# Kernel optimization log

Measured on AMD Instinct MI355X. Metric: run time of the kernel, lower is better.

## Reference

```python
import jax, jax.numpy as jnp
import numpy as np

B, S, D, H = 16, 1024, 768, 12
HD = D // H  # head_dim = 64

def setup_inputs() -> dict:
    key = jax.random.key(0)
    ks = jax.random.split(key, 6)
    s = 1.0 / np.sqrt(D)
    return {
        "z": jax.random.normal(ks[0], (B, S, D), dtype=jnp.float32),
        "W_q": jax.random.normal(ks[1], (D, D), dtype=jnp.float32) * s,
        "W_k": jax.random.normal(ks[2], (D, D), dtype=jnp.float32) * s,
        "W_v": jax.random.normal(ks[3], (D, D), dtype=jnp.float32) * s,
        "W_o": jax.random.normal(ks[4], (D, D), dtype=jnp.float32) * s,
        "b_o": jax.random.normal(ks[5], (D,), dtype=jnp.float32) * s,
    }

def reference(z, W_q, W_k, W_v, W_o, b_o):
    batch, seq, _ = z.shape
    # torch Linear: y = x @ W.T
    q = (z @ W_q.T).reshape(batch, seq, H, HD).transpose(0, 2, 1, 3)  # [B,H,S,hd]
    k = (z @ W_k.T).reshape(batch, seq, H, HD).transpose(0, 2, 1, 3)
    v = (z @ W_v.T).reshape(batch, seq, H, HD).transpose(0, 2, 1, 3)
    scores = jnp.einsum("bhqd,bhkd->bhqk", q, k) / np.sqrt(HD)
    attn = jax.nn.softmax(scores, axis=-1)
    ctx = jnp.einsum("bhqk,bhkd->bhqd", attn, v)  # [B,H,S,hd]
    ctx = ctx.transpose(0, 2, 1, 3).reshape(batch, seq, D)
    return ctx @ W_o.T + b_o
```

## Files before the change

kernel.cpp:

```cpp
#include <hip/hip_runtime.h>
#include <hip/hip_bf16.h>


typedef __attribute__((ext_vector_type(4))) float f32x4;
typedef __attribute__((ext_vector_type(16))) float f32x16;
typedef __attribute__((ext_vector_type(8))) __bf16 bf16x8;
typedef __attribute__((ext_vector_type(4))) unsigned int u32x4;

#if __has_builtin(__builtin_amdgcn_exp2f)
#define EXP2F __builtin_amdgcn_exp2f
#else
#define EXP2F exp2f
#endif

__device__ __forceinline__ unsigned short f2bf(float f) {
  union { float f; unsigned u; } v; v.f = f;
  unsigned r = v.u + 0x7FFFu + ((v.u >> 16) & 1u);
  return (unsigned short)(r >> 16);
}

__device__ __forceinline__ unsigned cvtpk(float a, float b) {
  unsigned r;
  asm("v_cvt_pk_bf16_f32 %0, %1, %2" : "=v"(r) : "v"(a), "v"(b));
  return r;
}

__device__ __forceinline__ void gl_lds16(const void* g, void* l) {
  __builtin_amdgcn_global_load_lds(
      (const __attribute__((address_space(1))) void*)g,
      (__attribute__((address_space(3))) void*)l, 16, 0, 0);
}

__global__ void cvt_f32_bf16(const float* __restrict__ in,
                             unsigned short* __restrict__ out, int n4) {
  int i = blockIdx.x * blockDim.x + threadIdx.x;
  int stride = gridDim.x * blockDim.x;
  for (; i < n4; i += stride) {
    float4 v = ((const float4*)in)[i];
    ushort4 o;
    o.x = f2bf(v.x); o.y = f2bf(v.y); o.z = f2bf(v.z); o.w = f2bf(v.w);
    ((ushort4*)out)[i] = o;
  }
}

__global__ void cvt4_f32_bf16(const float* __restrict__ i0, const float* __restrict__ i1,
                              const float* __restrict__ i2, const float* __restrict__ i3,
                              unsigned short* __restrict__ o0, unsigned short* __restrict__ o1,
                              unsigned short* __restrict__ o2, unsigned short* __restrict__ o3,
                              int n4) {
  const float* in = (blockIdx.y == 0) ? i0 : (blockIdx.y == 1) ? i1 : (blockIdx.y == 2) ? i2 : i3;
  unsigned short* out = (blockIdx.y == 0) ? o0 : (blockIdx.y == 1) ? o1 : (blockIdx.y == 2) ? o2 : o3;
  int i = blockIdx.x * blockDim.x + threadIdx.x;
  int stride = gridDim.x * blockDim.x;
  for (; i < n4; i += stride) {
    float4 v = ((const float4*)in)[i];
    ushort4 o;
    o.x = f2bf(v.x); o.y = f2bf(v.y); o.z = f2bf(v.z); o.w = f2bf(v.w);
    ((ushort4*)out)[i] = o;
  }
}

__global__ __launch_bounds__(256) void qkv_gemm(
    const unsigned short* __restrict__ A,
    const unsigned short* __restrict__ Wq,
    const unsigned short* __restrict__ Wk,
    const unsigned short* __restrict__ Wv,
    unsigned short* __restrict__ Qo,
    unsigned short* __restrict__ Ko,
    unsigned short* __restrict__ Vt) {
  __shared__ unsigned short As[2][128 * 64];
  __shared__ unsigned short Bs[2][128 * 64];
  const int bid = blockIdx.x;
  const int xcd = bid & 7, slot = bid >> 3;
  const int mt = xcd * 16 + slot / 18;
  const int rem = slot % 18;
  const int which = rem / 6;
  const int nt = rem % 6;
  const unsigned short* __restrict__ W =
      (which == 0) ? Wq : (which == 1) ? Wk : Wv;
  const int m0 = mt * 128;
  const int n0 = nt * 128;
  const int tid = threadIdx.x;
  const int lane = tid & 63;
  const int l15 = lane & 15, lg = lane >> 4;
  const int w = tid >> 6;
  const int wm = (w >> 1) * 64, wn = (w & 1) * 64;

  const int srow = tid >> 3;
  const int scg8 = (((tid & 7) ^ (srow & 7)) << 3);

#define QSTAGE(bi, kt)                                                         \
  do {                                                                         \
    _Pragma("unroll") for (int it = 0; it < 4; ++it) {                         \
      int row = srow + it * 32;                                                \
      int dst = (row * 8 + (tid & 7)) * 8;                                     \
      gl_lds16(A + (size_t)(m0 + row) * 768 + (kt) + scg8, &As[bi][dst]);      \
      gl_lds16(W + (size_t)(n0 + row) * 768 + (kt) + scg8, &Bs[bi][dst]);      \
    }                                                                          \
  } while (0)

  f32x4 acc[4][4] = {};
  const int rxf = l15 & 7;

  QSTAGE(0, 0);
  for (int kt = 0; kt < 768; kt += 64) {
    const int cur = (kt >> 6) & 1;
    if (kt < 704) {
      QSTAGE(cur ^ 1, kt + 64);
      asm volatile("s_waitcnt vmcnt(8)" ::: "memory");
    } else {
      asm volatile("s_waitcnt vmcnt(0)" ::: "memory");
    }
    __builtin_amdgcn_s_barrier();
    __builtin_amdgcn_sched_barrier(0);
#pragma unroll
    for (int kk = 0; kk < 64; kk += 32) {
      const int g0 = kk >> 3;
      bf16x8 a[4], b[4];
#pragma unroll
      for (int i = 0; i < 4; ++i)
        a[i] = *(const bf16x8*)&As[cur][(wm + i * 16 + l15) * 64 + (((g0 + lg) ^ rxf) << 3)];
#pragma unroll
      for (int j = 0; j < 4; ++j)
        b[j] = *(const bf16x8*)&Bs[cur][(wn + j * 16 + l15) * 64 + (((g0 + lg) ^ rxf) << 3)];
#pragma unroll
      for (int i = 0; i < 4; ++i)
#pragma unroll
        for (int j = 0; j < 4; ++j)
          acc[i][j] = __builtin_amdgcn_mfma_f32_16x16x32_bf16(
              a[i], b[j], acc[i][j], 0, 0, 0);
    }
    asm volatile("s_waitcnt lgkmcnt(0)" ::: "memory");
    __builtin_amdgcn_sched_barrier(0);
    __builtin_amdgcn_s_barrier();
  }

  if (which < 2) {
    unsigned short* __restrict__ O = which == 0 ? Qo : Ko;
    const float scl = which == 0 ? 0.125f * 1.44269504088896f : 1.0f;
#pragma unroll
    for (int i = 0; i < 4; ++i)
#pragma unroll
      for (int j = 0; j < 4; ++j)
#pragma unroll
        for (int r = 0; r < 4; ++r) {
          int row = m0 + wm + i * 16 + lg * 4 + r;
          int col = n0 + wn + j * 16 + l15;
          O[(size_t)row * 768 + col] = f2bf(acc[i][j][r] * scl);
        }
  } else {
#pragma unroll
    for (int i = 0; i < 4; ++i)
#pragma unroll
      for (int j = 0; j < 4; ++j) {
        int m = m0 + wm + i * 16 + lg * 4;
        int bb = m >> 10, s = m & 1023;
        int col = n0 + wn + j * 16 + l15;
        size_t off = ((size_t)(bb * 12 + (col >> 6)) * 64 + (col & 63)) * 1024 + s;
        ushort4 pk;
        pk.x = f2bf(acc[i][j][0]);
        pk.y = f2bf(acc[i][j][1]);
        pk.z = f2bf(acc[i][j][2]);
        pk.w = f2bf(acc[i][j][3]);
        *(ushort4*)(Vt + off) = pk;
      }
  }
#undef QSTAGE
}

__global__ __launch_bounds__(256, 2) void attn_fwd(
    const unsigned short* __restrict__ Q,
    const unsigned short* __restrict__ K,
    const unsigned short* __restrict__ Vt,
    unsigned short* __restrict__ ctx) {
  __shared__ unsigned short Ks[4][64 * 64];
  __shared__ unsigned short Vs[4][64 * 64];
  const int wg = blockIdx.x;
  const int xcd = wg & 7, slot = wg >> 3;
  const int bh = xcd * 24 + (slot >> 2);
  const int qt = slot & 3;
  const int b = bh / 12, h = bh - b * 12;

  const int tid = threadIdx.x;
  const int lane = tid & 63;
  const int l31 = lane & 31;
  const int hi = lane >> 5;
  const int w = tid >> 6;
  const int qbase = qt * 256 + w * 64;

  const size_t qkoff = (size_t)b * (1024 * 768) + h * 64;
  const size_t vtoff = (size_t)bh * (64 * 1024);

  const int sc = lane & 7;
  const int srsub = lane >> 3;
  const int scg = sc ^ srsub;
  const int srow0 = w * 16 + srsub;

  const unsigned short* k0 = K + qkoff + scg * 8 + (size_t)srow0 * 768;
  const unsigned short* k1 = k0 + 8 * 768;
  const unsigned short* v0 = Vt + vtoff + scg * 8 + (size_t)srow0 * 1024;
  const unsigned short* v1 = v0 + 8 * 1024;
  const int d0 = srow0 * 64 + sc * 8;
  const int d1 = d0 + 8 * 64;

#define STAGE(bi)                                                              \
  do {                                                                         \
    gl_lds16(k0, &Ks[bi][d0]);                                                 \
    gl_lds16(k1, &Ks[bi][d1]);                                                 \
    gl_lds16(v0, &Vs[bi][d0]);                                                 \
    gl_lds16(v1, &Vs[bi][d1]);                                                 \
    k0 += 64 * 768; k1 += 64 * 768; v0 += 64; v1 += 64;                        \
  } while (0)

  bf16x8 bqA[4], bqB[4];
  const unsigned short* Qp = Q + qkoff + (size_t)(qbase + l31) * 768 + hi * 8;
#pragma unroll
  for (int ks = 0; ks < 4; ++ks) {
    bqA[ks] = *(const bf16x8*)(Qp + ks * 16);
    bqB[ks] = *(const bf16x8*)(Qp + 32 * 768 + ks * 16);
  }

  f32x16 oA0 = {}, oA1 = {}, oB0 = {}, oB1 = {};
  float laccA[8] = {}, laccB[8] = {};

  const int rxor = l31 & 7;

#define ATTN_BODY(buf)                                                         \
  do {                                                                         \
    bf16x8 ak[2][4], bv[2][4];                                                 \
    _Pragma("unroll") for (int kb2 = 0; kb2 < 2; ++kb2)                        \
      _Pragma("unroll") for (int ks = 0; ks < 4; ++ks)                         \
        ak[kb2][ks] = *(const bf16x8*)&Ks[buf][(kb2 * 32 + l31) * 64 +         \
                                               (((ks * 2 + hi) ^ rxor) * 8)];  \
    _Pragma("unroll") for (int db = 0; db < 2; ++db)                           \
      _Pragma("unroll") for (int ks = 0; ks < 4; ++ks)                         \
        bv[db][ks] = *(const bf16x8*)&Vs[buf][(db * 32 + l31) * 64 +           \
                                              (((ks * 2 + hi) ^ rxor) * 8)];   \
    f32x16 sA0 = {}, sA1 = {}, sB0 = {}, sB1 = {};                             \
    __builtin_amdgcn_s_setprio(1);                                             \
    _Pragma("unroll") for (int ks = 0; ks < 4; ++ks) {                         \
      sA0 = __builtin_amdgcn_mfma_f32_32x32x16_bf16(ak[0][ks], bqA[ks], sA0, 0, 0, 0); \
      sA1 = __builtin_amdgcn_mfma_f32_32x32x16_bf16(ak[1][ks], bqA[ks], sA1, 0, 0, 0); \
    }                                                                          \
    _Pragma("unroll") for (int ks = 0; ks < 4; ++ks) {                         \
      sB0 = __builtin_amdgcn_mfma_f32_32x32x16_bf16(ak[0][ks], bqB[ks], sB0, 0, 0, 0); \
      sB1 = __builtin_amdgcn_mfma_f32_32x32x16_bf16(ak[1][ks], bqB[ks], sB1, 0, 0, 0); \
    }                                                                          \
    __builtin_amdgcn_s_setprio(0);                                             \
    _Pragma("unroll") for (int r = 0; r < 16; ++r) sA0[r] = EXP2F(sA0[r]);     \
    _Pragma("unroll") for (int r = 0; r < 16; ++r) sA1[r] = EXP2F(sA1[r]);     \
    _Pragma("unroll") for (int r = 0; r < 8; ++r)                              \
      laccA[r] += (sA0[r] + sA0[r + 8]) + (sA1[r] + sA1[r + 8]);               \
    bf16x8 pa[4];                                                              \
    _Pragma("unroll") for (int ks = 0; ks < 4; ++ks) {                         \
      f32x16 ps = (ks < 2) ? sA0 : sA1;                                        \
      const int roff = (ks & 1) * 8;                                           \
      unsigned c01 = cvtpk(ps[roff + 0], ps[roff + 1]);                        \
      unsigned c23 = cvtpk(ps[roff + 2], ps[roff + 3]);                        \
      unsigned c45 = cvtpk(ps[roff + 4], ps[roff + 5]);                        \
      unsigned c67 = cvtpk(ps[roff + 6], ps[roff + 7]);                        \
      unsigned e1 = hi ? c01 : c45;                                            \
      unsigned e2 = hi ? c23 : c67;                                            \
      unsigned se1 = (unsigned)__shfl_xor((int)e1, 32);                        \
      unsigned se2 = (unsigned)__shfl_xor((int)e2, 32);                        \
      u32x4 uw;                                                                \
      uw[0] = hi ? se1 : c01;                                                  \
      uw[1] = hi ? se2 : c23;                                                  \
      uw[2] = hi ? c45 : se1;                                                  \
      uw[3] = hi ? c67 : se2;                                                  \
      pa[ks] = __builtin_bit_cast(bf16x8, uw);                                 \
    }                                                                          \
    __builtin_amdgcn_s_setprio(1);                                             \
    _Pragma("unroll") for (int ks = 0; ks < 4; ++ks) {                         \
      oA0 = __builtin_amdgcn_mfma_f32_32x32x16_bf16(pa[ks], bv[0][ks], oA0, 0, 0, 0); \
      oA1 = __builtin_amdgcn_mfma_f32_32x32x16_bf16(pa[ks], bv[1][ks], oA1, 0, 0, 0); \
    }                                                                          \
    __builtin_amdgcn_s_setprio(0);                                             \
    _Pragma("unroll") for (int r = 0; r < 16; ++r) sB0[r] = EXP2F(sB0[r]);     \
    _Pragma("unroll") for (int r = 0; r < 16; ++r) sB1[r] = EXP2F(sB1[r]);     \
    _Pragma("unroll") for (int r = 0; r < 8; ++r)                              \
      laccB[r] += (sB0[r] + sB0[r + 8]) + (sB1[r] + sB1[r + 8]);               \
    _Pragma("unroll") for (int ks = 0; ks < 4; ++ks) {                         \
      f32x16 ps = (ks < 2) ? sB0 : sB1;                                        \
      const int roff = (ks & 1) * 8;                                           \
      unsigned c01 = cvtpk(ps[roff + 0], ps[roff + 1]);                        \
      unsigned c23 = cvtpk(ps[roff + 2], ps[roff + 3]);                        \
      unsigned c45 = cvtpk(ps[roff + 4], ps[roff + 5]);                        \
      unsigned c67 = cvtpk(ps[roff + 6], ps[roff + 7]);                        \
      unsigned e1 = hi ? c01 : c45;                                            \
      unsigned e2 = hi ? c23 : c67;                                            \
      unsigned se1 = (unsigned)__shfl_xor((int)e1, 32);                        \
      unsigned se2 = (unsigned)__shfl_xor((int)e2, 32);                        \
      u32x4 uw;                                                                \
      uw[0] = hi ? se1 : c01;                                                  \
      uw[1] = hi ? se2 : c23;                                                  \
      uw[2] = hi ? c45 : se1;                                                  \
      uw[3] = hi ? c67 : se2;                                                  \
      pa[ks] = __builtin_bit_cast(bf16x8, uw);                                 \
    }                                                                          \
    __builtin_amdgcn_s_setprio(1);                                             \
    _Pragma("unroll") for (int ks = 0; ks < 4; ++ks) {                         \
      oB0 = __builtin_amdgcn_mfma_f32_32x32x16_bf16(pa[ks], bv[0][ks], oB0, 0, 0, 0); \
      oB1 = __builtin_amdgcn_mfma_f32_32x32x16_bf16(pa[ks], bv[1][ks], oB1, 0, 0, 0); \
    }                                                                          \
    __builtin_amdgcn_s_setprio(0);                                             \
  } while (0)

  STAGE(0);
  STAGE(1);

#pragma unroll 1
  for (int i = 0; i < 8; ++i) {
    const int cur0 = (i & 1) * 2;
    if (i < 7) {
      STAGE(cur0 ^ 2);
      STAGE((cur0 ^ 2) + 1);
      asm volatile("s_waitcnt vmcnt(8)" ::: "memory");
    } else {
      asm volatile("s_waitcnt vmcnt(0)" ::: "memory");
    }
    __builtin_amdgcn_s_barrier();
    __builtin_amdgcn_sched_barrier(0);

    ATTN_BODY(cur0);
    ATTN_BODY(cur0 + 1);

    asm volatile("s_waitcnt lgkmcnt(0)" ::: "memory");
    __builtin_amdgcn_sched_barrier(0);
    __builtin_amdgcn_s_barrier();
  }

  unsigned short* Cp = ctx + qkoff;
  {
    float lsA = ((laccA[0] + laccA[1]) + (laccA[2] + laccA[3])) +
                ((laccA[4] + laccA[5]) + (laccA[6] + laccA[7]));
    lsA += __shfl_xor(lsA, 32);
    float invA = 1.0f / lsA;
#pragma unroll
    for (int r = 0; r < 16; ++r) {
      int qof = (r & 3) + 8 * (r >> 2) + 4 * hi;
      float invO = __shfl(invA, qof);
      size_t rowo = (size_t)(qbase + qof) * 768 + l31;
      Cp[rowo] = f2bf(oA0[r] * invO);
      Cp[rowo + 32] = f2bf(oA1[r] * invO);
    }
  }
  {
    float lsB = ((laccB[0] + laccB[1]) + (laccB[2] + laccB[3])) +
                ((laccB[4] + laccB[5]) + (laccB[6] + laccB[7]));
    lsB += __shfl_xor(lsB, 32);
    float invB = 1.0f / lsB;
#pragma unroll
    for (int r = 0; r < 16; ++r) {
      int qof = (r & 3) + 8 * (r >> 2) + 4 * hi;
      float invO = __shfl(invB, qof);
      size_t rowo = (size_t)(qbase + 32 + qof) * 768 + l31;
      Cp[rowo] = f2bf(oB0[r] * invO);
      Cp[rowo + 32] = f2bf(oB1[r] * invO);
    }
  }
#undef STAGE
#undef ATTN_BODY
}

__global__ __launch_bounds__(256) void oproj_gemm(
    const unsigned short* __restrict__ A,
    const unsigned short* __restrict__ W,
    const float* __restrict__ bias,
    float* __restrict__ out) {
  __shared__ unsigned short As[2][128 * 64];
  __shared__ unsigned short Bs[2][128 * 64];
  const int bid = blockIdx.x;
  const int xcd = bid & 7, slot = bid >> 3;
  const int mt = xcd * 16 + slot / 6;
  const int nt = slot % 6;
  const int m0 = mt * 128;
  const int n0 = nt * 128;
  const int tid = threadIdx.x;
  const int lane = tid & 63;
  const int l15 = lane & 15, lg = lane >> 4;
  const int w = tid >> 6;
  const int wm = (w >> 1) * 64, wn = (w & 1) * 64;

  const int srow = tid >> 3;
  const int scg8 = (((tid & 7) ^ (srow & 7)) << 3);

#define OSTAGE(bi, kt)                                                         \
  do {                                                                         \
    _Pragma("unroll") for (int it = 0; it < 4; ++it) {                         \
      int row = srow + it * 32;                                                \
      int dst = (row * 8 + (tid & 7)) * 8;                                     \
      gl_lds16(A + (size_t)(m0 + row) * 768 + (kt) + scg8, &As[bi][dst]);      \
      gl_lds16(W + (size_t)(n0 + row) * 768 + (kt) + scg8, &Bs[bi][dst]);      \
    }                                                                          \
  } while (0)

  f32x4 acc[4][4] = {};
  const int rxf = l15 & 7;

  OSTAGE(0, 0);
  for (int kt = 0; kt < 768; kt += 64) {
    const int cur = (kt >> 6) & 1;
    if (kt < 704) {
      OSTAGE(cur ^ 1, kt + 64);
      asm volatile("s_waitcnt vmcnt(8)" ::: "memory");
    } else {
      asm volatile("s_waitcnt vmcnt(0)" ::: "memory");
    }
    __builtin_amdgcn_s_barrier();
    __builtin_amdgcn_sched_barrier(0);
#pragma unroll
    for (int kk = 0; kk < 64; kk += 32) {
      const int g0 = kk >> 3;
      bf16x8 a[4], b[4];
#pragma unroll
      for (int i = 0; i < 4; ++i)
        a[i] = *(const bf16x8*)&As[cur][(wm + i * 16 + l15) * 64 + (((g0 + lg) ^ rxf) << 3)];
#pragma unroll
      for (int j = 0; j < 4; ++j)
        b[j] = *(const bf16x8*)&Bs[cur][(wn + j * 16 + l15) * 64 + (((g0 + lg) ^ rxf) << 3)];
#pragma unroll
      for (int i = 0; i < 4; ++i)
#pragma unroll
        for (int j = 0; j < 4; ++j)
          acc[i][j] = __builtin_amdgcn_mfma_f32_16x16x32_bf16(
              a[i], b[j], acc[i][j], 0, 0, 0);
    }
    asm volatile("s_waitcnt lgkmcnt(0)" ::: "memory");
    __builtin_amdgcn_sched_barrier(0);
    __builtin_amdgcn_s_barrier();
  }

#pragma unroll
  for (int i = 0; i < 4; ++i)
#pragma unroll
    for (int j = 0; j < 4; ++j)
#pragma unroll
      for (int r = 0; r < 4; ++r) {
        int row = m0 + wm + i * 16 + lg * 4 + r;
        int col = n0 + wn + j * 16 + l15;
        out[(size_t)row * 768 + col] = acc[i][j][r] + bias[col];
      }
#undef OSTAGE
}

extern "C" void kernel_launch(void* const* d_in, const int* in_sizes, int n_in,
                              void* d_out, int out_size, void* d_ws, size_t ws_size,
                              hipStream_t stream) {
  const float* z = (const float*)d_in[0];
  const float* Wq = (const float*)d_in[1];
  const float* Wk = (const float*)d_in[2];
  const float* Wv = (const float*)d_in[3];
  const float* Wo = (const float*)d_in[4];
  const float* bo = (const float*)d_in[5];
  float* out = (float*)d_out;

  const size_t NZ = (size_t)16 * 1024 * 768;
  const size_t NW = (size_t)768 * 768;

  unsigned short* zb = (unsigned short*)d_ws;
  unsigned short* Wqb = zb + NZ;
  unsigned short* Wkb = Wqb + NW;
  unsigned short* Wvb = Wkb + NW;
  unsigned short* Wob = Wvb + NW;
  unsigned short* Qb = Wob + NW;
  unsigned short* Kb = Qb + NZ;
  unsigned short* Vtb = Kb + NZ;
  unsigned short* Cb = Vtb + NZ;

  cvt_f32_bf16<<<2048, 256, 0, stream>>>(z, zb, (int)(NZ / 4));
  cvt4_f32_bf16<<<dim3(144, 4), 256, 0, stream>>>(Wq, Wk, Wv, Wo, Wqb, Wkb, Wvb, Wob,
                                                  (int)(NW / 4));

  qkv_gemm<<<2304, 256, 0, stream>>>(zb, Wqb, Wkb, Wvb, Qb, Kb, Vtb);
  attn_fwd<<<768, 256, 0, stream>>>(Qb, Kb, Vtb, Cb);
  oproj_gemm<<<768, 256, 0, stream>>>(Cb, Wob, bo, out);
}
```

Baseline: 184.3 us.

## Restructure attention into single-wave workgroups with one-buffer K/V staging

```diff
diff --git a/kernel.cpp b/kernel.cpp
--- a/kernel.cpp
+++ b/kernel.cpp
@@ -168,25 +168,23 @@
 #undef QSTAGE
 }
 
-__global__ __launch_bounds__(256, 2) void attn_fwd(
+__global__ __launch_bounds__(64) void attn_fwd(
     const unsigned short* __restrict__ Q,
     const unsigned short* __restrict__ K,
     const unsigned short* __restrict__ Vt,
     unsigned short* __restrict__ ctx) {
-  __shared__ unsigned short Ks[4][64 * 64];
-  __shared__ unsigned short Vs[4][64 * 64];
+  __shared__ unsigned short Ks[64 * 64];
+  __shared__ unsigned short Vs[64 * 64];
   const int wg = blockIdx.x;
   const int xcd = wg & 7, slot = wg >> 3;
-  const int bh = xcd * 24 + (slot >> 2);
-  const int qt = slot & 3;
+  const int bh = xcd * 24 + (slot >> 4);
+  const int unit = slot & 15;
   const int b = bh / 12, h = bh - b * 12;
 
-  const int tid = threadIdx.x;
-  const int lane = tid & 63;
+  const int lane = threadIdx.x & 63;
   const int l31 = lane & 31;
   const int hi = lane >> 5;
-  const int w = tid >> 6;
-  const int qbase = qt * 256 + w * 64;
+  const int qbase = unit * 64;
 
   const size_t qkoff = (size_t)b * (1024 * 768) + h * 64;
   const size_t vtoff = (size_t)bh * (64 * 1024);
@@ -194,22 +192,17 @@
   const int sc = lane & 7;
   const int srsub = lane >> 3;
   const int scg = sc ^ srsub;
-  const int srow0 = w * 16 + srsub;
-
-  const unsigned short* k0 = K + qkoff + scg * 8 + (size_t)srow0 * 768;
-  const unsigned short* k1 = k0 + 8 * 768;
-  const unsigned short* v0 = Vt + vtoff + scg * 8 + (size_t)srow0 * 1024;
-  const unsigned short* v1 = v0 + 8 * 1024;
-  const int d0 = srow0 * 64 + sc * 8;
-  const int d1 = d0 + 8 * 64;
-
-#define STAGE(bi)                                                              \
+  const unsigned short* kp = K + qkoff + scg * 8 + (size_t)srsub * 768;
+  const unsigned short* vp = Vt + vtoff + scg * 8 + (size_t)srsub * 1024;
+  const int dbase = srsub * 64 + sc * 8;
+
+#define STAGE()                                                                \
   do {                                                                         \
-    gl_lds16(k0, &Ks[bi][d0]);                                                 \
-    gl_lds16(k1, &Ks[bi][d1]);                                                 \
-    gl_lds16(v0, &Vs[bi][d0]);                                                 \
-    gl_lds16(v1, &Vs[bi][d1]);                                                 \
-    k0 += 64 * 768; k1 += 64 * 768; v0 += 64; v1 += 64;                        \
+    _Pragma("unroll") for (int j = 0; j < 8; ++j) {                            \
+      gl_lds16(kp + (size_t)j * (8 * 768), &Ks[dbase + j * (8 * 64)]);         \
+      gl_lds16(vp + (size_t)j * (8 * 1024), &Vs[dbase + j * (8 * 64)]);        \
+    }                                                                          \
+    kp += 64 * 768; vp += 64;                                                  \
   } while (0)
 
   bf16x8 bqA[4], bqB[4];
@@ -225,109 +218,92 @@
 
   const int rxor = l31 & 7;
 
-#define ATTN_BODY(buf)                                                         \
+#define BODY32(AK, BV)                                                         \
   do {                                                                         \
-    bf16x8 ak[2][4], bv[2][4];                                                 \
-    _Pragma("unroll") for (int kb2 = 0; kb2 < 2; ++kb2)                        \
-      _Pragma("unroll") for (int ks = 0; ks < 4; ++ks)                         \
-        ak[kb2][ks] = *(const bf16x8*)&Ks[buf][(kb2 * 32 + l31) * 64 +         \
-                                               (((ks * 2 + hi) ^ rxor) * 8)];  \
-    _Pragma("unroll") for (int db = 0; db < 2; ++db)                           \
-      _Pragma("unroll") for (int ks = 0; ks < 4; ++ks)                         \
-        bv[db][ks] = *(const bf16x8*)&Vs[buf][(db * 32 + l31) * 64 +           \
-                                              (((ks * 2 + hi) ^ rxor) * 8)];   \
-    f32x16 sA0 = {}, sA1 = {}, sB0 = {}, sB1 = {};                             \
+    f32x16 sA = {}, sB = {};                                                   \
     __builtin_amdgcn_s_setprio(1);                                             \
     _Pragma("unroll") for (int ks = 0; ks < 4; ++ks) {                         \
-      sA0 = __builtin_amdgcn_mfma_f32_32x32x16_bf16(ak[0][ks], bqA[ks], sA0, 0, 0, 0); \
-      sA1 = __builtin_amdgcn_mfma_f32_32x32x16_bf16(ak[1][ks], bqA[ks], sA1, 0, 0, 0); \
-    }                                                                          \
-    _Pragma("unroll") for (int ks = 0; ks < 4; ++ks) {                         \
-      sB0 = __builtin_amdgcn_mfma_f32_32x32x16_bf16(ak[0][ks], bqB[ks], sB0, 0, 0, 0); \
-      sB1 = __builtin_amdgcn_mfma_f32_32x32x16_bf16(ak[1][ks], bqB[ks], sB1, 0, 0, 0); \
+      sA = __builtin_amdgcn_mfma_f32_32x32x16_bf16(AK[ks], bqA[ks], sA, 0, 0, 0); \
+      sB = __builtin_amdgcn_mfma_f32_32x32x16_bf16(AK[ks], bqB[ks], sB, 0, 0, 0); \
     }                                                                          \
     __builtin_amdgcn_s_setprio(0);                                             \
-    _Pragma("unroll") for (int r = 0; r < 16; ++r) sA0[r] = EXP2F(sA0[r]);     \
-    _Pragma("unroll") for (int r = 0; r < 16; ++r) sA1[r] = EXP2F(sA1[r]);     \
-    _Pragma("unroll") for (int r = 0; r < 8; ++r)                              \
-      laccA[r] += (sA0[r] + sA0[r + 8]) + (sA1[r] + sA1[r + 8]);               \
-    bf16x8 pa[4];                                                              \
-    _Pragma("unroll") for (int ks = 0; ks < 4; ++ks) {                         \
-      f32x16 ps = (ks < 2) ? sA0 : sA1;                                        \
-      const int roff = (ks & 1) * 8;                                           \
-      unsigned c01 = cvtpk(ps[roff + 0], ps[roff + 1]);                        \
-      unsigned c23 = cvtpk(ps[roff + 2], ps[roff + 3]);                        \
-      unsigned c45 = cvtpk(ps[roff + 4], ps[roff + 5]);                        \
-      unsigned c67 = cvtpk(ps[roff + 6], ps[roff + 7]);                        \
-      unsigned e1 = hi ? c01 : c45;                                            \
-      unsigned e2 = hi ? c23 : c67;                                            \
-      unsigned se1 = (unsigned)__shfl_xor((int)e1, 32);                        \
-      unsigned se2 = (unsigned)__shfl_xor((int)e2, 32);                        \
-      u32x4 uw;                                                                \
-      uw[0] = hi ? se1 : c01;                                                  \
-      uw[1] = hi ? se2 : c23;                                                  \
-      uw[2] = hi ? c45 : se1;                                                  \
-      uw[3] = hi ? c67 : se2;                                                  \
-      pa[ks] = __builtin_bit_cast(bf16x8, uw);                                 \
+    _Pragma("unroll") for (int r = 0; r < 16; ++r) sA[r] = EXP2F(sA[r]);       \
+    _Pragma("unroll") for (int r = 0; r < 16; ++r) sB[r] = EXP2F(sB[r]);       \
+    _Pragma("unroll") for (int r = 0; r < 8; ++r) {                            \
+      laccA[r] += sA[r] + sA[r + 8];                                           \
+      laccB[r] += sB[r] + sB[r + 8];                                           \
+    }                                                                          \
+    bf16x8 paA[2], paB[2];                                                     \
+    _Pragma("unroll") for (int ks = 0; ks < 2; ++ks) {                         \
+      const int roff = ks * 8;                                                 \
+      unsigned a01 = cvtpk(sA[roff + 0], sA[roff + 1]);                        \
+      unsigned a23 = cvtpk(sA[roff + 2], sA[roff + 3]);                        \
+      unsigned a45 = cvtpk(sA[roff + 4], sA[roff + 5]);                        \
+      unsigned a67 = cvtpk(sA[roff + 6], sA[roff + 7]);                        \
+      unsigned ae1 = hi ? a01 : a45;                                           \
+      unsigned ae2 = hi ? a23 : a67;                                           \
+      unsigned as1 = (unsigned)__shfl_xor((int)ae1, 32);                       \
+      unsigned as2 = (unsigned)__shfl_xor((int)ae2, 32);                       \
+      u32x4 uwa;                                                               \
+      uwa[0] = hi ? as1 : a01;                                                 \
+      uwa[1] = hi ? as2 : a23;                                                 \
+      uwa[2] = hi ? a45 : as1;                                                 \
+      uwa[3] = hi ? a67 : as2;                                                 \
+      paA[ks] = __builtin_bit_cast(bf16x8, uwa);                               \
+      unsigned b01 = cvtpk(sB[roff + 0], sB[roff + 1]);                        \
+      unsigned b23 = cvtpk(sB[roff + 2], sB[roff + 3]);                        \
+      unsigned b45 = cvtpk(sB[roff + 4], sB[roff + 5]);                        \
+      unsigned b67 = cvtpk(sB[roff + 6], sB[roff + 7]);                        \
+      unsigned be1 = hi ? b01 : b45;                                           \
+      unsigned be2 = hi ? b23 : b67;                                           \
+      unsigned bs1 = (unsigned)__shfl_xor((int)be1, 32);                       \
+      unsigned bs2 = (unsigned)__shfl_xor((int)be2, 32);                       \
+      u32x4 uwb;                                                               \
+      uwb[0] = hi ? bs1 : b01;                                                 \
+      uwb[1] = hi ? bs2 : b23;                                                 \
+      uwb[2] = hi ? b45 : bs1;                                                 \
+      uwb[3] = hi ? b67 : bs2;                                                 \
+      paB[ks] = __builtin_bit_cast(bf16x8, uwb);                               \
     }                                                                          \
     __builtin_amdgcn_s_setprio(1);                                             \
-    _Pragma("unroll") for (int ks = 0; ks < 4; ++ks) {                         \
-      oA0 = __builtin_amdgcn_mfma_f32_32x32x16_bf16(pa[ks], bv[0][ks], oA0, 0, 0, 0); \
-      oA1 = __builtin_amdgcn_mfma_f32_32x32x16_bf16(pa[ks], bv[1][ks], oA1, 0, 0, 0); \
-    }                                                                          \
-    __builtin_amdgcn_s_setprio(0);                                             \
-    _Pragma("unroll") for (int r = 0; r < 16; ++r) sB0[r] = EXP2F(sB0[r]);     \
-    _Pragma("unroll") for (int r = 0; r < 16; ++r) sB1[r] = EXP2F(sB1[r]);     \
-    _Pragma("unroll") for (int r = 0; r < 8; ++r)                              \
-      laccB[r] += (sB0[r] + sB0[r + 8]) + (sB1[r] + sB1[r + 8]);               \
-    _Pragma("unroll") for (int ks = 0; ks < 4; ++ks) {                         \
-      f32x16 ps = (ks < 2) ? sB0 : sB1;                                        \
-      const int roff = (ks & 1) * 8;                                           \
-      unsigned c01 = cvtpk(ps[roff + 0], ps[roff + 1]);                        \
-      unsigned c23 = cvtpk(ps[roff + 2], ps[roff + 3]);                        \
-      unsigned c45 = cvtpk(ps[roff + 4], ps[roff + 5]);                        \
-      unsigned c67 = cvtpk(ps[roff + 6], ps[roff + 7]);                        \
-      unsigned e1 = hi ? c01 : c45;                                            \
-      unsigned e2 = hi ? c23 : c67;                                            \
-      unsigned se1 = (unsigned)__shfl_xor((int)e1, 32);                        \
-      unsigned se2 = (unsigned)__shfl_xor((int)e2, 32);                        \
-      u32x4 uw;                                                                \
-      uw[0] = hi ? se1 : c01;                                                  \
-      uw[1] = hi ? se2 : c23;                                                  \
-      uw[2] = hi ? c45 : se1;                                                  \
-      uw[3] = hi ? c67 : se2;                                                  \
-      pa[ks] = __builtin_bit_cast(bf16x8, uw);                                 \
-    }                                                                          \
-    __builtin_amdgcn_s_setprio(1);                                             \
-    _Pragma("unroll") for (int ks = 0; ks < 4; ++ks) {                         \
-      oB0 = __builtin_amdgcn_mfma_f32_32x32x16_bf16(pa[ks], bv[0][ks], oB0, 0, 0, 0); \
-      oB1 = __builtin_amdgcn_mfma_f32_32x32x16_bf16(pa[ks], bv[1][ks], oB1, 0, 0, 0); \
+    _Pragma("unroll") for (int ks = 0; ks < 2; ++ks) {                         \
+      oA0 = __builtin_amdgcn_mfma_f32_32x32x16_bf16(paA[ks], BV[0][ks], oA0, 0, 0, 0); \
+      oA1 = __builtin_amdgcn_mfma_f32_32x32x16_bf16(paA[ks], BV[1][ks], oA1, 0, 0, 0); \
+      oB0 = __builtin_amdgcn_mfma_f32_32x32x16_bf16(paB[ks], BV[0][ks], oB0, 0, 0, 0); \
+      oB1 = __builtin_amdgcn_mfma_f32_32x32x16_bf16(paB[ks], BV[1][ks], oB1, 0, 0, 0); \
     }                                                                          \
     __builtin_amdgcn_s_setprio(0);                                             \
   } while (0)
 
-  STAGE(0);
-  STAGE(1);
+  STAGE();
+  asm volatile("s_waitcnt vmcnt(0)" ::: "memory");
 
 #pragma unroll 1
-  for (int i = 0; i < 8; ++i) {
-    const int cur0 = (i & 1) * 2;
-    if (i < 7) {
-      STAGE(cur0 ^ 2);
-      STAGE((cur0 ^ 2) + 1);
-      asm volatile("s_waitcnt vmcnt(8)" ::: "memory");
-    } else {
-      asm volatile("s_waitcnt vmcnt(0)" ::: "memory");
-    }
-    __builtin_amdgcn_s_barrier();
-    __builtin_amdgcn_sched_barrier(0);
-
-    ATTN_BODY(cur0);
-    ATTN_BODY(cur0 + 1);
-
+  for (int i = 0; i < 16; ++i) {
+    bf16x8 akL[4], akH[4], bvL[2][2], bvH[2][2];
+#pragma unroll
+    for (int ks = 0; ks < 4; ++ks) {
+      akL[ks] = *(const bf16x8*)&Ks[l31 * 64 + (((ks * 2 + hi) ^ rxor) * 8)];
+      akH[ks] = *(const bf16x8*)&Ks[(32 + l31) * 64 + (((ks * 2 + hi) ^ rxor) * 8)];
+    }
+#pragma unroll
+    for (int db = 0; db < 2; ++db)
+#pragma unroll
+      for (int k2 = 0; k2 < 2; ++k2) {
+        bvL[db][k2] = *(const bf16x8*)&Vs[(db * 32 + l31) * 64 + (((k2 * 2 + hi) ^ rxor) * 8)];
+        bvH[db][k2] = *(const bf16x8*)&Vs[(db * 32 + l31) * 64 + (((k2 * 2 + 4 + hi) ^ rxor) * 8)];
+      }
     asm volatile("s_waitcnt lgkmcnt(0)" ::: "memory");
     __builtin_amdgcn_sched_barrier(0);
-    __builtin_amdgcn_s_barrier();
+
+    if (i < 15) STAGE();
+
+    BODY32(akL, bvL);
+    BODY32(akH, bvH);
+
+    if (i < 15) {
+      asm volatile("s_waitcnt vmcnt(0)" ::: "memory");
+    }
   }
 
   unsigned short* Cp = ctx + qkoff;
@@ -360,7 +336,7 @@
     }
   }
 #undef STAGE
-#undef ATTN_BODY
+#undef BODY32
 }
 
 __global__ __launch_bounds__(256) void oproj_gemm(
@@ -473,6 +449,6 @@
                                                   (int)(NW / 4));
 
   qkv_gemm<<<2304, 256, 0, stream>>>(zb, Wqb, Wkb, Wvb, Qb, Kb, Vtb);
-  attn_fwd<<<768, 256, 0, stream>>>(Qb, Kb, Vtb, Cb);
+  attn_fwd<<<3072, 64, 0, stream>>>(Qb, Kb, Vtb, Cb);
   oproj_gemm<<<768, 256, 0, stream>>>(Cb, Wob, bo, out);
 }
```

New measurement: 209.5 us. 13.7% more time.
